# Optimization experiments

Measured on AMD Instinct MI355X. Metric: run time of the kernel, lower is better.

## Reference

```python
import jax, jax.numpy as jnp
import numpy as np

BN_EPS = 1e-5


def setup_inputs() -> dict:
    key = jax.random.key(0)
    ks = jax.random.split(key, 8)
    B, C_IN, C_OUT, N, K = 4, 32, 64, 32768, 16
    feature = jax.random.normal(ks[0], (B, C_IN, N), dtype=jnp.float32)
    knn_inds = jax.random.randint(ks[1], (B, N, K), 0, N, dtype=jnp.int64)
    W1 = jax.random.normal(ks[2], (C_OUT, C_IN), dtype=jnp.float32) * 0.05
    W2 = jax.random.normal(ks[3], (C_OUT, C_IN), dtype=jnp.float32) * 0.05
    bn_gamma = jax.random.uniform(ks[4], (2 * C_OUT,), dtype=jnp.float32) + 0.5
    bn_beta = jax.random.normal(ks[5], (2 * C_OUT,), dtype=jnp.float32) * 0.1
    bn_mean = jax.random.normal(ks[6], (2 * C_OUT,), dtype=jnp.float32) * 0.1
    bn_var = jax.random.uniform(ks[7], (2 * C_OUT,), dtype=jnp.float32) + 0.5
    return {"feature": feature, "knn_inds": knn_inds, "W1": W1, "W2": W2,
            "bn_gamma": bn_gamma, "bn_beta": bn_beta, "bn_mean": bn_mean, "bn_var": bn_var}


def reference(feature, knn_inds, W1, W2, bn_gamma, bn_beta, bn_mean, bn_var):
    B, C_in, N = feature.shape
    K = knn_inds.shape[2]
    # 1x1 Conv1d == per-point GEMM
    local = jnp.einsum('oc,bcn->bon', W1, feature)   # (B, C_out, N)
    edge = jnp.einsum('oc,bcn->bon', W2, feature)    # (B, C_out, N)
    C = local.shape[1]
    # KNN gather: neighbour[b,c,n,j] = edge[b,c,knn_inds[b,n,j]]
    idx = knn_inds.reshape(B, 1, N * K)              # broadcast over channel dim
    neighbour = jnp.take_along_axis(edge, idx, axis=2).reshape(B, C, N, K)
    central = local[:, :, :, None]                   # (B, C, N, 1)
    diff = neighbour - central
    ef = jnp.concatenate([jnp.broadcast_to(central, (B, C, N, K)), diff], axis=1)  # (B, 2C, N, K)
    # BatchNorm2d (eval mode: running stats) + ReLU
    inv = (bn_gamma / jnp.sqrt(bn_var + BN_EPS)).reshape(1, 2 * C, 1, 1)
    shift = (bn_beta - bn_mean * bn_gamma / jnp.sqrt(bn_var + BN_EPS)).reshape(1, 2 * C, 1, 1)
    ef = jax.nn.relu(ef * inv + shift)
    return jnp.mean(ef, axis=3)                      # (B, 2C, N)
```

## Files before the change

### kernel.cpp

```cpp
#include <hip/hip_runtime.h>
#include <hip/hip_fp16.h>

#define CIN 32
#define COUT 64
#define NB 4
#define NPTS 32768
#define KNN 16

typedef unsigned short u16;
typedef _Float16 h2 __attribute__((ext_vector_type(2)));

__device__ __forceinline__ u16 f2h(float f) {
  _Float16 h = (_Float16)f;
  u16 u; __builtin_memcpy(&u, &h, 2); return u;
}
__device__ __forceinline__ h2 u2h2(unsigned int u) {
  h2 h; __builtin_memcpy(&h, &u, 4); return h;
}
__device__ __forceinline__ unsigned int h22u(h2 h) {
  unsigned int u; __builtin_memcpy(&u, &h, 4); return u;
}

__global__ __launch_bounds__(256) void k1_gemm(
    const float* __restrict__ feat, const float* __restrict__ W1,
    const float* __restrict__ W2, const float* __restrict__ gamma,
    const float* __restrict__ beta, const float* __restrict__ mean,
    const float* __restrict__ var, u16* __restrict__ lt, u16* __restrict__ et,
    float* __restrict__ out) {
  const int bid = blockIdx.x;
  const int b = bid >> 9;
  const int n0 = (bid & 511) << 6;
  const int t = threadIdx.x;
  const int lane = t & 63;
  const int wchunk = __builtin_amdgcn_readfirstlane(t >> 6);
  const int n = n0 + lane;

  float f[CIN];
  const float* fp = feat + (size_t)b * CIN * NPTS + n;
#pragma unroll
  for (int c = 0; c < CIN; ++c) f[c] = fp[(size_t)c * NPTS];

  const int half = wchunk >> 1;
  const int rbase = (wchunk & 1) * 32;
  const float* Wp = half ? W2 : W1;
  u16* dst = half ? et : lt;

  unsigned int pk[16];

#pragma unroll
  for (int oo = 0; oo < 32; oo += 4) {
    const float* w0 = Wp + (size_t)(rbase + oo) * CIN;
    float a0 = 0.f, a1 = 0.f, a2 = 0.f, a3 = 0.f;
#pragma unroll
    for (int c = 0; c < CIN; ++c) {
      const float fc = f[c];
      a0 = fmaf(w0[c], fc, a0);
      a1 = fmaf(w0[CIN + c], fc, a1);
      a2 = fmaf(w0[2 * CIN + c], fc, a2);
      a3 = fmaf(w0[3 * CIN + c], fc, a3);
    }
    pk[oo / 2]     = (unsigned)f2h(a0) | ((unsigned)f2h(a1) << 16);
    pk[oo / 2 + 1] = (unsigned)f2h(a2) | ((unsigned)f2h(a3) << 16);
    if (half == 0) {
      const float acc[4] = {a0, a1, a2, a3};
#pragma unroll
      for (int i = 0; i < 4; ++i) {
        const int r = rbase + oo + i;
        const float iv = gamma[r] * rsqrtf(var[r] + 1e-5f);
        const float sh = beta[r] - mean[r] * iv;
        out[((size_t)b * 128 + r) * NPTS + n] = fmaxf(fmaf(acc[i], iv, sh), 0.f);
      }
    }
  }
  uint4* dp = reinterpret_cast<uint4*>(dst + ((size_t)(b * NPTS + n)) * COUT + rbase);
#pragma unroll
  for (int q = 0; q < 4; ++q)
    dp[q] = make_uint4(pk[4 * q], pk[4 * q + 1], pk[4 * q + 2], pk[4 * q + 3]);
}

__global__ __launch_bounds__(256) void k2_gather(
    const u16* __restrict__ lt, const u16* __restrict__ et,
    const int* __restrict__ knn, const float* __restrict__ gamma,
    const float* __restrict__ beta, const float* __restrict__ mean,
    const float* __restrict__ var, float* __restrict__ out) {
  __shared__ float obuf[64 * 17];
  int bid = blockIdx.x;
  bid = (bid & 7) * 1024 + (bid >> 3);
  const int b = bid >> 11;
  const int n0 = (bid & 2047) << 4;
  const int t = threadIdx.x;
  const int w = t >> 6;
  const int lane = t & 63;
  const int kg = lane >> 3;
  const int cg = lane & 7;
  const int ch = cg * 8;

  h2 inv_h2[4], sh_h2[4];
#pragma unroll
  for (int i = 0; i < 4; ++i) {
    const int r0 = 64 + ch + 2 * i;
    const float iv0 = gamma[r0] * rsqrtf(var[r0] + 1e-5f);
    const float iv1 = gamma[r0 + 1] * rsqrtf(var[r0 + 1] + 1e-5f);
    const float s0 = beta[r0] - mean[r0] * iv0;
    const float s1 = beta[r0 + 1] - mean[r0 + 1] * iv1;
    inv_h2[i] = (h2){(_Float16)iv0, (_Float16)iv1};
    sh_h2[i] = (h2){(_Float16)s0, (_Float16)s1};
  }

  const size_t rowbase = (size_t)b * NPTS;
  const u16* etb = et + rowbase * COUT + ch;
  const u16* ltb = lt + rowbase * COUT + ch;

  int i0[4], i1[4];
  uint4 lv[4], e0[4], e1[4];
#pragma unroll
  for (int it = 0; it < 4; ++it) {
    const int n = n0 + w * 4 + it;
    const int* kp = knn + (rowbase + n) * KNN;
    i0[it] = kp[kg];
    i1[it] = kp[kg + 8];
    lv[it] = *reinterpret_cast<const uint4*>(ltb + (size_t)n * COUT);
  }
#pragma unroll
  for (int it = 0; it < 4; ++it) {
    e0[it] = *reinterpret_cast<const uint4*>(etb + ((size_t)i0[it] << 6));
    e1[it] = *reinterpret_cast<const uint4*>(etb + ((size_t)i1[it] << 6));
  }

  const h2 zero = (h2){(_Float16)0.f, (_Float16)0.f};
#pragma unroll
  for (int it = 0; it < 4; ++it) {
    const int nn = w * 4 + it;
    const unsigned int* lu = reinterpret_cast<const unsigned int*>(&lv[it]);
    const unsigned int* a0 = reinterpret_cast<const unsigned int*>(&e0[it]);
    const unsigned int* a1 = reinterpret_cast<const unsigned int*>(&e1[it]);
    unsigned int accu[4];
#pragma unroll
    for (int i = 0; i < 4; ++i) {
      const h2 tt = sh_h2[i] - u2h2(lu[i]) * inv_h2[i];
      h2 acc = __builtin_elementwise_max(u2h2(a0[i]) * inv_h2[i] + tt, zero);
      acc = acc + __builtin_elementwise_max(u2h2(a1[i]) * inv_h2[i] + tt, zero);
      accu[i] = h22u(acc);
    }
#pragma unroll
    for (int i = 0; i < 4; ++i) {
      unsigned int v = accu[i];
      v = h22u(u2h2(v) + u2h2((unsigned)__shfl_xor((int)v, 8)));
      v = h22u(u2h2(v) + u2h2((unsigned)__shfl_xor((int)v, 16)));
      v = h22u(u2h2(v) + u2h2((unsigned)__shfl_xor((int)v, 32)));
      accu[i] = v;
    }
    if (kg == 0) {
      const float inv16 = 0.0625f;
#pragma unroll
      for (int i = 0; i < 4; ++i) {
        const h2 fv = u2h2(accu[i]);
        obuf[(ch + 2 * i) * 17 + nn] = (float)fv.x * inv16;
        obuf[(ch + 2 * i + 1) * 17 + nn] = (float)fv.y * inv16;
      }
    }
  }
  __syncthreads();
  const int c = t >> 2;
  const int nn4 = (t & 3) * 4;
  float4 v = make_float4(obuf[c * 17 + nn4], obuf[c * 17 + nn4 + 1],
                         obuf[c * 17 + nn4 + 2], obuf[c * 17 + nn4 + 3]);
  *reinterpret_cast<float4*>(out + ((size_t)b * 128 + 64 + c) * NPTS + n0 + nn4) = v;
}

extern "C" void kernel_launch(void* const* d_in, const int* in_sizes, int n_in,
                              void* d_out, int out_size, void* d_ws, size_t ws_size,
                              hipStream_t stream) {
  const float* feat  = (const float*)d_in[0];
  const int*   knn   = (const int*)d_in[1];
  const float* W1    = (const float*)d_in[2];
  const float* W2    = (const float*)d_in[3];
  const float* gamma = (const float*)d_in[4];
  const float* beta  = (const float*)d_in[5];
  const float* mean  = (const float*)d_in[6];
  const float* var   = (const float*)d_in[7];
  float* out = (float*)d_out;

  u16* lt = (u16*)d_ws;
  u16* et = lt + (size_t)NB * NPTS * COUT;

  k1_gemm<<<dim3(NB * NPTS / 64), 256, 0, stream>>>(feat, W1, W2, gamma, beta,
                                                    mean, var, lt, et, out);
  k2_gather<<<dim3(NB * NPTS / 16), 256, 0, stream>>>(lt, et, knn, gamma, beta,
                                                      mean, var, out);
}
```

Measured before the change: 64.71 us.

## Store edge features as FP8, remap gather threads, use packed fp32 math

The edge-feature table written by the GEMM kernel changes from fp16 to fp8 (e4m3), which halves the bytes fetched in the random neighbour gather. The gather kernel is remapped so each lane owns one point and 8 channels and loops over all 16 neighbours with fp32 packed math. This removes the cross-lane shuffle reduction and moves each block to 32 points. The GEMM also switches to packed fp32 FMAs. The cost is fp8 quantisation error in the neighbour values, which may threaten tolerance, and more registers per lane for 16 outstanding gathers.

```diff
diff --git a/kernel.cpp b/kernel.cpp
--- a/kernel.cpp
+++ b/kernel.cpp
@@ -8,24 +8,25 @@
 #define KNN 16
 
 typedef unsigned short u16;
-typedef _Float16 h2 __attribute__((ext_vector_type(2)));
+typedef unsigned char u8;
+typedef float f2v __attribute__((ext_vector_type(2)));
 
 __device__ __forceinline__ u16 f2h(float f) {
   _Float16 h = (_Float16)f;
   u16 u; __builtin_memcpy(&u, &h, 2); return u;
 }
-__device__ __forceinline__ h2 u2h2(unsigned int u) {
-  h2 h; __builtin_memcpy(&h, &u, 4); return h;
-}
-__device__ __forceinline__ unsigned int h22u(h2 h) {
-  unsigned int u; __builtin_memcpy(&u, &h, 4); return u;
+__device__ __forceinline__ f2v h2_to_f2(unsigned int u) {
+  _Float16 a, b;
+  __builtin_memcpy(&a, (const char*)&u, 2);
+  __builtin_memcpy(&b, ((const char*)&u) + 2, 2);
+  return (f2v){(float)a, (float)b};
 }
 
 __global__ __launch_bounds__(256) void k1_gemm(
     const float* __restrict__ feat, const float* __restrict__ W1,
     const float* __restrict__ W2, const float* __restrict__ gamma,
     const float* __restrict__ beta, const float* __restrict__ mean,
-    const float* __restrict__ var, u16* __restrict__ lt, u16* __restrict__ et,
+    const float* __restrict__ var, u16* __restrict__ lt, u8* __restrict__ et,
     float* __restrict__ out) {
   const int bid = blockIdx.x;
   const int b = bid >> 9;
@@ -35,33 +36,40 @@
   const int wchunk = __builtin_amdgcn_readfirstlane(t >> 6);
   const int n = n0 + lane;
 
-  float f[CIN];
+  f2v fv[16];
   const float* fp = feat + (size_t)b * CIN * NPTS + n;
 #pragma unroll
-  for (int c = 0; c < CIN; ++c) f[c] = fp[(size_t)c * NPTS];
+  for (int c2 = 0; c2 < 16; ++c2)
+    fv[c2] = (f2v){fp[(size_t)(2 * c2) * NPTS], fp[(size_t)(2 * c2 + 1) * NPTS]};
 
   const int half = wchunk >> 1;
   const int rbase = (wchunk & 1) * 32;
   const float* Wp = half ? W2 : W1;
-  u16* dst = half ? et : lt;
 
-  unsigned int pk[16];
+  unsigned int pkh[16];
+  unsigned int pk8[8];
 
 #pragma unroll
   for (int oo = 0; oo < 32; oo += 4) {
     const float* w0 = Wp + (size_t)(rbase + oo) * CIN;
-    float a0 = 0.f, a1 = 0.f, a2 = 0.f, a3 = 0.f;
+    const f2v* wr0 = reinterpret_cast<const f2v*>(w0);
+    const f2v* wr1 = reinterpret_cast<const f2v*>(w0 + CIN);
+    const f2v* wr2 = reinterpret_cast<const f2v*>(w0 + 2 * CIN);
+    const f2v* wr3 = reinterpret_cast<const f2v*>(w0 + 3 * CIN);
+    f2v p0 = (f2v)0.f, p1 = (f2v)0.f, p2 = (f2v)0.f, p3 = (f2v)0.f;
 #pragma unroll
-    for (int c = 0; c < CIN; ++c) {
-      const float fc = f[c];
-      a0 = fmaf(w0[c], fc, a0);
-      a1 = fmaf(w0[CIN + c], fc, a1);
-      a2 = fmaf(w0[2 * CIN + c], fc, a2);
-      a3 = fmaf(w0[3 * CIN + c], fc, a3);
+    for (int c2 = 0; c2 < 16; ++c2) {
+      const f2v fc = fv[c2];
+      p0 = __builtin_elementwise_fma(wr0[c2], fc, p0);
+      p1 = __builtin_elementwise_fma(wr1[c2], fc, p1);
+      p2 = __builtin_elementwise_fma(wr2[c2], fc, p2);
+      p3 = __builtin_elementwise_fma(wr3[c2], fc, p3);
     }
-    pk[oo / 2]     = (unsigned)f2h(a0) | ((unsigned)f2h(a1) << 16);
-    pk[oo / 2 + 1] = (unsigned)f2h(a2) | ((unsigned)f2h(a3) << 16);
+    const float a0 = p0.x + p0.y, a1 = p1.x + p1.y;
+    const float a2 = p2.x + p2.y, a3 = p3.x + p3.y;
     if (half == 0) {
+      pkh[oo / 2]     = (unsigned)f2h(a0) | ((unsigned)f2h(a1) << 16);
+      pkh[oo / 2 + 1] = (unsigned)f2h(a2) | ((unsigned)f2h(a3) << 16);
       const float acc[4] = {a0, a1, a2, a3};
 #pragma unroll
       for (int i = 0; i < 4; ++i) {
@@ -70,102 +78,101 @@
         const float sh = beta[r] - mean[r] * iv;
         out[((size_t)b * 128 + r) * NPTS + n] = fmaxf(fmaf(acc[i], iv, sh), 0.f);
       }
+    } else {
+      int u = 0;
+      u = __builtin_amdgcn_cvt_pk_fp8_f32(a0, a1, u, false);
+      u = __builtin_amdgcn_cvt_pk_fp8_f32(a2, a3, u, true);
+      pk8[oo / 4] = (unsigned)u;
     }
   }
-  uint4* dp = reinterpret_cast<uint4*>(dst + ((size_t)(b * NPTS + n)) * COUT + rbase);
+  if (half == 0) {
+    uint4* dp = reinterpret_cast<uint4*>(lt + ((size_t)(b * NPTS + n)) * COUT + rbase);
 #pragma unroll
-  for (int q = 0; q < 4; ++q)
-    dp[q] = make_uint4(pk[4 * q], pk[4 * q + 1], pk[4 * q + 2], pk[4 * q + 3]);
+    for (int q = 0; q < 4; ++q)
+      dp[q] = make_uint4(pkh[4 * q], pkh[4 * q + 1], pkh[4 * q + 2], pkh[4 * q + 3]);
+  } else {
+    uint4* dp = reinterpret_cast<uint4*>(et + ((size_t)(b * NPTS + n)) * COUT + rbase);
+    dp[0] = make_uint4(pk8[0], pk8[1], pk8[2], pk8[3]);
+    dp[1] = make_uint4(pk8[4], pk8[5], pk8[6], pk8[7]);
+  }
 }
 
 __global__ __launch_bounds__(256) void k2_gather(
-    const u16* __restrict__ lt, const u16* __restrict__ et,
+    const u16* __restrict__ lt, const u8* __restrict__ et,
     const int* __restrict__ knn, const float* __restrict__ gamma,
     const float* __restrict__ beta, const float* __restrict__ mean,
     const float* __restrict__ var, float* __restrict__ out) {
-  __shared__ float obuf[64 * 17];
+  __shared__ float obuf[64 * 33];
   int bid = blockIdx.x;
-  bid = (bid & 7) * 1024 + (bid >> 3);
-  const int b = bid >> 11;
-  const int n0 = (bid & 2047) << 4;
+  bid = (bid & 7) * 512 + (bid >> 3);
+  const int b = bid >> 10;
+  const int n_blk = (bid & 1023) << 5;
   const int t = threadIdx.x;
   const int w = t >> 6;
   const int lane = t & 63;
-  const int kg = lane >> 3;
+  const int nn = lane >> 3;
   const int cg = lane & 7;
   const int ch = cg * 8;
 
-  h2 inv_h2[4], sh_h2[4];
+  f2v inv[4], sh[4];
 #pragma unroll
   for (int i = 0; i < 4; ++i) {
     const int r0 = 64 + ch + 2 * i;
     const float iv0 = gamma[r0] * rsqrtf(var[r0] + 1e-5f);
     const float iv1 = gamma[r0 + 1] * rsqrtf(var[r0 + 1] + 1e-5f);
-    const float s0 = beta[r0] - mean[r0] * iv0;
-    const float s1 = beta[r0 + 1] - mean[r0 + 1] * iv1;
-    inv_h2[i] = (h2){(_Float16)iv0, (_Float16)iv1};
-    sh_h2[i] = (h2){(_Float16)s0, (_Float16)s1};
+    inv[i] = (f2v){iv0, iv1};
+    sh[i] = (f2v){beta[r0] - mean[r0] * iv0, beta[r0 + 1] - mean[r0 + 1] * iv1};
   }
 
+  const int n = n_blk + w * 8 + nn;
   const size_t rowbase = (size_t)b * NPTS;
-  const u16* etb = et + rowbase * COUT + ch;
-  const u16* ltb = lt + rowbase * COUT + ch;
 
-  int i0[4], i1[4];
-  uint4 lv[4], e0[4], e1[4];
+  const int4* kp = reinterpret_cast<const int4*>(knn + (rowbase + n) * KNN);
+  const int4 kv0 = kp[0], kv1 = kp[1], kv2 = kp[2], kv3 = kp[3];
+  const uint4 lv = *reinterpret_cast<const uint4*>(lt + (rowbase + n) * COUT + ch);
+
+  const u8* etb = et + rowbase * COUT + ch;
+  uint2 e[16];
+  const int idx[16] = {kv0.x, kv0.y, kv0.z, kv0.w, kv1.x, kv1.y, kv1.z, kv1.w,
+                       kv2.x, kv2.y, kv2.z, kv2.w, kv3.x, kv3.y, kv3.z, kv3.w};
 #pragma unroll
-  for (int it = 0; it < 4; ++it) {
-    const int n = n0 + w * 4 + it;
-    const int* kp = knn + (rowbase + n) * KNN;
-    i0[it] = kp[kg];
-    i1[it] = kp[kg + 8];
-    lv[it] = *reinterpret_cast<const uint4*>(ltb + (size_t)n * COUT);
-  }
+  for (int k = 0; k < 16; ++k)
+    e[k] = *reinterpret_cast<const uint2*>(etb + ((size_t)idx[k] << 6));
+
+  const unsigned int* lu = reinterpret_cast<const unsigned int*>(&lv);
+  f2v tt[4];
 #pragma unroll
-  for (int it = 0; it < 4; ++it) {
-    e0[it] = *reinterpret_cast<const uint4*>(etb + ((size_t)i0[it] << 6));
-    e1[it] = *reinterpret_cast<const uint4*>(etb + ((size_t)i1[it] << 6));
+  for (int i = 0; i < 4; ++i) tt[i] = sh[i] - h2_to_f2(lu[i]) * inv[i];
+
+  f2v acc[4] = {(f2v)0.f, (f2v)0.f, (f2v)0.f, (f2v)0.f};
+  const f2v zero = (f2v)0.f;
+#pragma unroll
+  for (int k = 0; k < 16; ++k) {
+    const f2v d0 = __builtin_amdgcn_cvt_pk_f32_fp8(e[k].x, false);
+    const f2v d1 = __builtin_amdgcn_cvt_pk_f32_fp8(e[k].x, true);
+    const f2v d2 = __builtin_amdgcn_cvt_pk_f32_fp8(e[k].y, false);
+    const f2v d3 = __builtin_amdgcn_cvt_pk_f32_fp8(e[k].y, true);
+    acc[0] += __builtin_elementwise_max(__builtin_elementwise_fma(d0, inv[0], tt[0]), zero);
+    acc[1] += __builtin_elementwise_max(__builtin_elementwise_fma(d1, inv[1], tt[1]), zero);
+    acc[2] += __builtin_elementwise_max(__builtin_elementwise_fma(d2, inv[2], tt[2]), zero);
+    acc[3] += __builtin_elementwise_max(__builtin_elementwise_fma(d3, inv[3], tt[3]), zero);
   }
 
-  const h2 zero = (h2){(_Float16)0.f, (_Float16)0.f};
+  const int ncol = w * 8 + nn;
 #pragma unroll
-  for (int it = 0; it < 4; ++it) {
-    const int nn = w * 4 + it;
-    const unsigned int* lu = reinterpret_cast<const unsigned int*>(&lv[it]);
-    const unsigned int* a0 = reinterpret_cast<const unsigned int*>(&e0[it]);
-    const unsigned int* a1 = reinterpret_cast<const unsigned int*>(&e1[it]);
-    unsigned int accu[4];
-#pragma unroll
-    for (int i = 0; i < 4; ++i) {
-      const h2 tt = sh_h2[i] - u2h2(lu[i]) * inv_h2[i];
-      h2 acc = __builtin_elementwise_max(u2h2(a0[i]) * inv_h2[i] + tt, zero);
-      acc = acc + __builtin_elementwise_max(u2h2(a1[i]) * inv_h2[i] + tt, zero);
-      accu[i] = h22u(acc);
-    }
-#pragma unroll
-    for (int i = 0; i < 4; ++i) {
-      unsigned int v = accu[i];
-      v = h22u(u2h2(v) + u2h2((unsigned)__shfl_xor((int)v, 8)));
-      v = h22u(u2h2(v) + u2h2((unsigned)__shfl_xor((int)v, 16)));
-      v = h22u(u2h2(v) + u2h2((unsigned)__shfl_xor((int)v, 32)));
-      accu[i] = v;
-    }
-    if (kg == 0) {
-      const float inv16 = 0.0625f;
-#pragma unroll
-      for (int i = 0; i < 4; ++i) {
-        const h2 fv = u2h2(accu[i]);
-        obuf[(ch + 2 * i) * 17 + nn] = (float)fv.x * inv16;
-        obuf[(ch + 2 * i + 1) * 17 + nn] = (float)fv.y * inv16;
-      }
-    }
+  for (int i = 0; i < 4; ++i) {
+    obuf[(ch + 2 * i) * 33 + ncol] = acc[i].x * 0.0625f;
+    obuf[(ch + 2 * i + 1) * 33 + ncol] = acc[i].y * 0.0625f;
   }
   __syncthreads();
-  const int c = t >> 2;
-  const int nn4 = (t & 3) * 4;
-  float4 v = make_float4(obuf[c * 17 + nn4], obuf[c * 17 + nn4 + 1],
-                         obuf[c * 17 + nn4 + 2], obuf[c * 17 + nn4 + 3]);
-  *reinterpret_cast<float4*>(out + ((size_t)b * 128 + 64 + c) * NPTS + n0 + nn4) = v;
+#pragma unroll
+  for (int r = 0; r < 2; ++r) {
+    const int c = (t >> 3) + (r << 5);
+    const int nn4 = (t & 7) * 4;
+    float4 v = make_float4(obuf[c * 33 + nn4], obuf[c * 33 + nn4 + 1],
+                           obuf[c * 33 + nn4 + 2], obuf[c * 33 + nn4 + 3]);
+    *reinterpret_cast<float4*>(out + ((size_t)b * 128 + 64 + c) * NPTS + n_blk + nn4) = v;
+  }
 }
 
 extern "C" void kernel_launch(void* const* d_in, const int* in_sizes, int n_in,
@@ -182,10 +189,10 @@
   float* out = (float*)d_out;
 
   u16* lt = (u16*)d_ws;
-  u16* et = lt + (size_t)NB * NPTS * COUT;
+  u8* et = (u8*)(lt + (size_t)NB * NPTS * COUT);
 
   k1_gemm<<<dim3(NB * NPTS / 64), 256, 0, stream>>>(feat, W1, W2, gamma, beta,
                                                     mean, var, lt, et, out);
-  k2_gather<<<dim3(NB * NPTS / 16), 256, 0, stream>>>(lt, et, knn, gamma, beta,
+  k2_gather<<<dim3(NB * NPTS / 32), 256, 0, stream>>>(lt, et, knn, gamma, beta,
                                                       mean, var, out);
 }
```

Measured after the change: 55.07 us. 1.17x faster.
